# Performance work log

Measured on AMD Instinct MI355X. Metric: run time of the kernel, lower is better.

The kernel has to match this reference:

```python
import jax, jax.numpy as jnp
import numpy as np

N = 100_000       # nodes
E = 1_600_000     # directed edges (avg degree 16)
IN, H, Z = 128, 128, 64


def setup_inputs() -> dict:
    key = jax.random.key(0)
    ks = jax.random.split(key, 8)
    x = jax.random.normal(ks[0], (N, IN), dtype=jnp.float32)
    edge_index = jax.random.randint(ks[1], (2, E), 0, N, dtype=jnp.int32)
    # Glorot-ish init like PyG GCNConv
    W1 = jax.random.normal(ks[2], (IN, H), dtype=jnp.float32) / np.sqrt(IN).astype(np.float32)
    b1 = jnp.zeros((H,), dtype=jnp.float32)
    Wmu = jax.random.normal(ks[3], (H, Z), dtype=jnp.float32) / np.sqrt(H).astype(np.float32)
    bmu = jnp.zeros((Z,), dtype=jnp.float32)
    Wlv = jax.random.normal(ks[4], (H, Z), dtype=jnp.float32) / np.sqrt(H).astype(np.float32)
    blv = jnp.zeros((Z,), dtype=jnp.float32)
    return {"x": x, "edge_index": edge_index, "W1": W1, "b1": b1,
            "Wmu": Wmu, "bmu": bmu, "Wlv": Wlv, "blv": blv}


def _gcn_conv(x, src, dst, norm, W, b):
    """PyG GCNConv: out = scatter_add(norm * (x @ W)[src], dst) + b."""
    h = x @ W                                   # [N, out_dim]
    msg = h[src] * norm[:, None]                # [E+N, out_dim] gather + scale
    out = jax.ops.segment_sum(msg, dst, num_segments=N)
    return out + b


def reference(x, edge_index, W1, b1, Wmu, bmu, Wlv, blv):
    loop = jnp.arange(N, dtype=edge_index.dtype)
    src = jnp.concatenate([edge_index[0], loop])   # add self-loops (PyG default)
    dst = jnp.concatenate([edge_index[1], loop])
    # symmetric normalization D^{-1/2} (A+I) D^{-1/2}
    deg = jax.ops.segment_sum(jnp.ones_like(dst, dtype=x.dtype), dst, num_segments=N)
    dinv = jax.lax.rsqrt(deg)                      # deg >= 1 thanks to self-loops
    norm = dinv[src] * dinv[dst]                   # [E+N]
    h = jax.nn.relu(_gcn_conv(x, src, dst, norm, W1, b1))
    mu = _gcn_conv(h, src, dst, norm, Wmu, bmu)
    logvar = _gcn_conv(h, src, dst, norm, Wlv, blv)
    return (mu, logvar)
```

## Files before the change

kernel.cpp:

```cpp
#include <hip/hip_runtime.h>
#include <hip/hip_bf16.h>
#include <stdint.h>

static inline size_t ws_align(size_t x) { return (x + 255) & ~(size_t)255; }

typedef __attribute__((ext_vector_type(8))) short bf16x8;
typedef __attribute__((ext_vector_type(4))) float f32x4;

__device__ __forceinline__ uint32_t pack_bf16(float a, float b) {
    uint32_t ua = __float_as_uint(a), ub = __float_as_uint(b);
    ua = (ua + 0x7fffu + ((ua >> 16) & 1u)) >> 16;
    ub = (ub + 0x7fffu + ((ub >> 16) & 1u)) >> 16;
    return ua | (ub << 16);
}
__device__ __forceinline__ uint16_t cvt_bf16(float a) {
    uint32_t ua = __float_as_uint(a);
    return (uint16_t)((ua + 0x7fffu + ((ua >> 16) & 1u)) >> 16);
}
__device__ __forceinline__ float bf_lo(uint32_t v) { return __uint_as_float(v << 16); }
__device__ __forceinline__ float bf_hi(uint32_t v) { return __uint_as_float(v & 0xffff0000u); }

__device__ __forceinline__ void fma8(float* acc, uint4 g, float wt) {
    acc[0] = fmaf(bf_lo(g.x), wt, acc[0]); acc[1] = fmaf(bf_hi(g.x), wt, acc[1]);
    acc[2] = fmaf(bf_lo(g.y), wt, acc[2]); acc[3] = fmaf(bf_hi(g.y), wt, acc[3]);
    acc[4] = fmaf(bf_lo(g.z), wt, acc[4]); acc[5] = fmaf(bf_hi(g.z), wt, acc[5]);
    acc[6] = fmaf(bf_lo(g.w), wt, acc[6]); acc[7] = fmaf(bf_hi(g.w), wt, acc[7]);
}

__global__ __launch_bounds__(256) void k_pre(const int* __restrict__ dst, int* __restrict__ cntAB,
                                             const float* __restrict__ x, uint32_t* __restrict__ xb,
                                             const float* __restrict__ W1,
                                             const float* __restrict__ Wmu, const float* __restrict__ Wlv,
                                             uint32_t* __restrict__ BtG1, uint32_t* __restrict__ BtG2,
                                             int E, int nchunk, int NB, int n4) {
    const int b = blockIdx.x;
    if (b < nchunk) {
        __shared__ int h[512];
        for (int t = threadIdx.x; t < NB; t += 256) h[t] = 0;
        __syncthreads();
        const int per = (E + nchunk - 1) / nchunk;
        const int e0 = b * per, e1 = (e0 + per < E) ? e0 + per : E;
        for (int e = e0 + threadIdx.x; e < e1; e += 256)
            atomicAdd(&h[dst[e] >> 8], 1);
        __syncthreads();
        for (int t = threadIdx.x; t < NB; t += 256) cntAB[t * nchunk + b] = h[t];
    } else if (b < nchunk + 34) {
        int t = (b - nchunk) * 256 + threadIdx.x;
        int c = t / 68, k2 = t % 68;
        uint32_t v = 0;
        if (k2 < 64) v = pack_bf16(W1[(2 * k2) * 128 + c], W1[(2 * k2 + 1) * 128 + c]);
        BtG1[t] = v;
    } else if (b < nchunk + 68) {
        int t = (b - nchunk - 34) * 256 + threadIdx.x;
        int c = t / 68, k2 = t % 68;
        uint32_t v = 0;
        if (k2 < 64) {
            const float* Wc = (c < 64) ? (Wmu + c) : (Wlv + (c - 64));
            v = pack_bf16(Wc[(2 * k2) * 64], Wc[(2 * k2 + 1) * 64]);
        }
        BtG2[t] = v;
    } else {
        int idx = (b - nchunk - 68) * 256 + threadIdx.x;
        if (idx < n4) {
            float4 v = ((const float4*)x)[idx];
            ((uint2*)xb)[idx] = make_uint2(pack_bf16(v.x, v.y), pack_bf16(v.z, v.w));
        }
    }
}

__global__ __launch_bounds__(256) void k_scan1(const int* __restrict__ cnt, int* __restrict__ rp,
                                               int* __restrict__ bsum, int N) {
    __shared__ int sh[256];
    int t = threadIdx.x;
    int base = blockIdx.x * 1024 + t * 4;
    int v[4];
#pragma unroll
    for (int i = 0; i < 4; i++) v[i] = (base + i < N) ? cnt[base + i] : 0;
    int s = v[0] + v[1] + v[2] + v[3];
    sh[t] = s;
    __syncthreads();
    for (int off = 1; off < 256; off <<= 1) {
        int x = (t >= off) ? sh[t - off] : 0;
        __syncthreads();
        sh[t] += x;
        __syncthreads();
    }
    int excl = sh[t] - s;
    if (t == 255) bsum[blockIdx.x] = sh[255];
    int run = excl;
#pragma unroll
    for (int i = 0; i < 4; i++) {
        if (base + i < N) rp[base + i] = run;
        run += v[i];
    }
}

__global__ __launch_bounds__(256) void k_scan2(int* __restrict__ bsum, int nb) {
    __shared__ int sh[256];
    int t = threadIdx.x;
    int v = (t < nb) ? bsum[t] : 0;
    sh[t] = v;
    __syncthreads();
    for (int off = 1; off < 256; off <<= 1) {
        int x = (t >= off) ? sh[t - off] : 0;
        __syncthreads();
        sh[t] += x;
        __syncthreads();
    }
    if (t < nb) bsum[t] = sh[t] - v;
}

__global__ void k_scan3(int* __restrict__ rp, const int* __restrict__ bsum, int N, int E) {
    int i = blockIdx.x * blockDim.x + threadIdx.x;
    if (i < N) rp[i] += bsum[i >> 10];
    if (i == N) rp[N] = E;
}

__global__ __launch_bounds__(256) void k_bscatter(const int* __restrict__ src, const int* __restrict__ dst,
                                                  const int* __restrict__ baseAB, uint2* __restrict__ ebkt,
                                                  int E, int nchunk, int NB) {
    __shared__ int bump[512];
    const int c = blockIdx.x;
    for (int t = threadIdx.x; t < NB; t += 256) bump[t] = baseAB[t * nchunk + c];
    __syncthreads();
    const int per = (E + nchunk - 1) / nchunk;
    const int e0 = c * per, e1 = (e0 + per < E) ? e0 + per : E;
    for (int e = e0 + threadIdx.x; e < e1; e += 256) {
        int d = dst[e], s = src[e];
        int pos = atomicAdd(&bump[d >> 8], 1);
        ebkt[pos] = make_uint2((uint32_t)s, (uint32_t)d);
    }
}

__global__ __launch_bounds__(256) void k_bbuild(const uint2* __restrict__ ebkt, const int* __restrict__ baseAB,
                                                float* __restrict__ dinv, int* __restrict__ rp,
                                                uint32_t* __restrict__ csrc, int nchunk, int N) {
    __shared__ int h[256];
    __shared__ int sh[256];
    __shared__ int rpd[256];
    __shared__ int fl[256];
    const int t = threadIdx.x;
    h[t] = 0;
    fl[t] = 0;
    __syncthreads();
    const int b = blockIdx.x;
    const int e0 = baseAB[b * nchunk], e1 = baseAB[(b + 1) * nchunk];
    for (int e = e0 + t; e < e1; e += 256)
        atomicAdd(&h[ebkt[e].y & 255], 1);
    __syncthreads();
    const int c = h[t];
    sh[t] = c;
    __syncthreads();
    for (int off = 1; off < 256; off <<= 1) {
        int x = (t >= off) ? sh[t - off] : 0;
        __syncthreads();
        sh[t] += x;
        __syncthreads();
    }
    rpd[t] = e0 + sh[t] - c;
    int node = (b << 8) + t;
    if (node < N) {
        rp[node] = rpd[t];
        dinv[node] = rsqrtf((float)(c + 1));
    }
    if (node == N - 1 || t == 255) {
        if (node + 1 <= N && (node == N - 1)) rp[N] = e0 + sh[255];
    }
    __syncthreads();
    for (int e = e0 + t; e < e1; e += 256) {
        uint2 sd = ebkt[e];
        int dl = (int)(sd.y & 255);
        int posL = atomicAdd(&fl[dl], 1);
        csrc[rpd[dl] + posL] = sd.x;
    }
}

__global__ __launch_bounds__(256) void k_agg(const uint8_t* __restrict__ featB,
                                             uint32_t* __restrict__ outB,
                                             const int* __restrict__ rp,
                                             const uint32_t* __restrict__ csrc,
                                             const float* __restrict__ dinv, int N) {
    int node = blockIdx.x * 4 + (threadIdx.x >> 6);
    if (node >= N) return;
    int lane = threadIdx.x & 63;
    int j = lane & 15;
    int q = lane >> 4;
    int beg = rp[node], end = rp[node + 1];
    float di = dinv[node];
    float w0 = (q == 0) ? di * di : 0.0f;
    const uint8_t* fb = featB + (size_t)j * 16;

    uint4 sv = *(const uint4*)(fb + (size_t)node * 256);
    float acc[8];
    acc[0] = bf_lo(sv.x) * w0; acc[1] = bf_hi(sv.x) * w0;
    acc[2] = bf_lo(sv.y) * w0; acc[3] = bf_hi(sv.y) * w0;
    acc[4] = bf_lo(sv.z) * w0; acc[5] = bf_hi(sv.z) * w0;
    acc[6] = bf_lo(sv.w) * w0; acc[7] = bf_hi(sv.w) * w0;

    for (int base = beg + q; base < end; base += 16) {
        bool v1 = base + 4 < end, v2 = base + 8 < end, v3 = base + 12 < end;
        uint32_t s0 = csrc[base];
        uint32_t s1 = v1 ? csrc[base + 4] : 0u;
        uint32_t s2 = v2 ? csrc[base + 8] : 0u;
        uint32_t s3 = v3 ? csrc[base + 12] : 0u;
        float wa = dinv[s0] * di;
        float wb = v1 ? dinv[s1] * di : 0.f;
        float wc = v2 ? dinv[s2] * di : 0.f;
        float wd = v3 ? dinv[s3] * di : 0.f;
        uint4 g0 = *(const uint4*)(fb + (size_t)s0 * 256);
        uint4 g1 = *(const uint4*)(fb + (size_t)s1 * 256);
        uint4 g2 = *(const uint4*)(fb + (size_t)s2 * 256);
        uint4 g3 = *(const uint4*)(fb + (size_t)s3 * 256);
        fma8(acc, g0, wa);
        fma8(acc, g1, wb);
        fma8(acc, g2, wc);
        fma8(acc, g3, wd);
    }

#pragma unroll
    for (int k = 0; k < 8; k++) {
        acc[k] += __shfl_xor(acc[k], 16, 64);
        acc[k] += __shfl_xor(acc[k], 32, 64);
    }
    if (q == 0) {
        uint4 p = make_uint4(pack_bf16(acc[0], acc[1]), pack_bf16(acc[2], acc[3]),
                             pack_bf16(acc[4], acc[5]), pack_bf16(acc[6], acc[7]));
        *(uint4*)(outB + (size_t)node * 64 + j * 4) = p;
    }
}

__global__ __launch_bounds__(256) void k_gemm1_mfma(
        const uint8_t* __restrict__ A, uint8_t* __restrict__ C,
        const uint32_t* __restrict__ BtG, const float* __restrict__ bias, int N) {
    __shared__ uint32_t Bt[128 * 68];
    for (int t = threadIdx.x; t < 128 * 68 / 4; t += 256)
        ((uint4*)Bt)[t] = ((const uint4*)BtG)[t];
    __syncthreads();

    const int lane = threadIdx.x & 63;
    const int wv = threadIdx.x >> 6;
    const int rrow = lane & 15;
    const int g = lane >> 4;
    const int r0 = blockIdx.x * 64 + wv * 16;
    const int rl = r0 + rrow;
    const int rc = (rl < N) ? rl : (N - 1);

    bf16x8 a[4];
    const uint8_t* arow = A + (size_t)rc * 256 + g * 16;
#pragma unroll
    for (int kb = 0; kb < 4; kb++) a[kb] = *(const bf16x8*)(arow + kb * 64);

    f32x4 acc[8];
#pragma unroll
    for (int ct = 0; ct < 8; ct++) acc[ct] = (f32x4){0.f, 0.f, 0.f, 0.f};

    const char* btb = (const char*)Bt;
#pragma unroll
    for (int ct = 0; ct < 8; ct++) {
        const char* bp = btb + (ct * 16 + rrow) * 272 + g * 16;
#pragma unroll
        for (int kb = 0; kb < 4; kb++) {
            bf16x8 bfr = *(const bf16x8*)(bp + kb * 64);
            acc[ct] = __builtin_amdgcn_mfma_f32_16x16x32_bf16(a[kb], bfr, acc[ct], 0, 0, 0);
        }
    }

#pragma unroll
    for (int ct = 0; ct < 8; ct++) {
        const int col = ct * 16 + rrow;
        const float bv = bias[col];
#pragma unroll
        for (int r = 0; r < 4; r++) {
            int row = r0 + g * 4 + r;
            if (row < N) {
                float h = fmaxf(acc[ct][r] + bv, 0.f);
                *(uint16_t*)(C + (size_t)row * 256 + col * 2) = cvt_bf16(h);
            }
        }
    }
}

__global__ __launch_bounds__(256) void k_gemm2_mfma(
        const uint8_t* __restrict__ A, float* __restrict__ out,
        const uint32_t* __restrict__ BtG,
        const float* __restrict__ bmu, const float* __restrict__ blv, int N) {
    __shared__ uint32_t Bt[128 * 68];
    for (int t = threadIdx.x; t < 128 * 68 / 4; t += 256)
        ((uint4*)Bt)[t] = ((const uint4*)BtG)[t];
    __syncthreads();

    const int lane = threadIdx.x & 63;
    const int wv = threadIdx.x >> 6;
    const int rrow = lane & 15;
    const int g = lane >> 4;
    const int r0 = blockIdx.x * 64 + wv * 16;
    const int rl = r0 + rrow;
    const int rc = (rl < N) ? rl : (N - 1);

    bf16x8 a[4];
    const uint8_t* arow = A + (size_t)rc * 256 + g * 16;
#pragma unroll
    for (int kb = 0; kb < 4; kb++) a[kb] = *(const bf16x8*)(arow + kb * 64);

    f32x4 acc[8];
#pragma unroll
    for (int ct = 0; ct < 8; ct++) acc[ct] = (f32x4){0.f, 0.f, 0.f, 0.f};

    const char* btb = (const char*)Bt;
#pragma unroll
    for (int ct = 0; ct < 8; ct++) {
        const char* bp = btb + (ct * 16 + rrow) * 272 + g * 16;
#pragma unroll
        for (int kb = 0; kb < 4; kb++) {
            bf16x8 bfr = *(const bf16x8*)(bp + kb * 64);
            acc[ct] = __builtin_amdgcn_mfma_f32_16x16x32_bf16(a[kb], bfr, acc[ct], 0, 0, 0);
        }
    }

#pragma unroll
    for (int ct = 0; ct < 8; ct++) {
        const int col = ct * 16 + rrow;
        const float bv = (col < 64) ? bmu[col] : blv[col - 64];
        float* obase = (col < 64) ? (out + col) : (out + (size_t)N * 64 + (col - 64));
#pragma unroll
        for (int r = 0; r < 4; r++) {
            int row = r0 + g * 4 + r;
            if (row < N) obase[(size_t)row * 64] = acc[ct][r] + bv;
        }
    }
}

extern "C" void kernel_launch(void* const* d_in, const int* in_sizes, int n_in,
                              void* d_out, int out_size, void* d_ws, size_t ws_size,
                              hipStream_t stream) {
    const float* x   = (const float*)d_in[0];
    const int*   ei  = (const int*)d_in[1];
    const float* W1  = (const float*)d_in[2];
    const float* b1  = (const float*)d_in[3];
    const float* Wmu = (const float*)d_in[4];
    const float* bmu = (const float*)d_in[5];
    const float* Wlv = (const float*)d_in[6];
    const float* blv = (const float*)d_in[7];
    float* out = (float*)d_out;

    const int N = in_sizes[0] / 128;
    const int E = in_sizes[1] / 2;
    const int* src = ei;
    const int* dst = ei + E;

    const int nchunk = 256;
    const int NB = (N + 255) >> 8;
    const int M = NB * nchunk;
    const int n4 = N * 32;

    char* ws = (char*)d_ws;
    size_t off = 0;
    float* dinv    = (float*)(ws + off);    off = ws_align(off + (size_t)N * 4);
    int* rp        = (int*)(ws + off);      off = ws_align(off + (size_t)(N + 1) * 4);
    int* bsum      = (int*)(ws + off);      off = ws_align(off + 1024 * 4);
    int* cntAB     = (int*)(ws + off);      off = ws_align(off + (size_t)(M + 64) * 4);
    int* baseAB    = (int*)(ws + off);      off = ws_align(off + (size_t)(M + 64) * 4);
    uint32_t* BtG1 = (uint32_t*)(ws + off); off = ws_align(off + 128 * 68 * 4);
    uint32_t* BtG2 = (uint32_t*)(ws + off); off = ws_align(off + 128 * 68 * 4);
    uint32_t* csrc = (uint32_t*)(ws + off); off = ws_align(off + (size_t)E * 4);
    uint32_t* xb   = (uint32_t*)(ws + off); off = ws_align(off + (size_t)N * 256);
    uint8_t* F1    = (uint8_t*)(ws + off);  off = ws_align(off + (size_t)N * 256);
    uint2* ebkt    = (uint2*)(ws + off);    off = ws_align(off + (size_t)E * 8);

    const int b = 256;
    const int ncvt = (n4 + 255) / 256;

    k_pre<<<nchunk + 68 + ncvt, 256, 0, stream>>>(dst, cntAB, x, xb, W1, Wmu, Wlv,
                                                  BtG1, BtG2, E, nchunk, NB, n4);
    k_scan1<<<(M + 1023) / 1024, 256, 0, stream>>>(cntAB, baseAB, bsum, M);
    k_scan2<<<1, 256, 0, stream>>>(bsum, (M + 1023) / 1024);
    k_scan3<<<(M + 1 + b - 1) / b, b, 0, stream>>>(baseAB, bsum, M, E);
    k_bscatter<<<nchunk, 256, 0, stream>>>(src, dst, baseAB, ebkt, E, nchunk, NB);
    k_bbuild<<<NB, 256, 0, stream>>>(ebkt, baseAB, dinv, rp, csrc, nchunk, N);

    const int aggBlocks = (N + 3) / 4;
    k_agg<<<aggBlocks, 256, 0, stream>>>((const uint8_t*)xb, (uint32_t*)F1, rp, csrc, dinv, N);
    k_gemm1_mfma<<<(N + 63) / 64, 256, 0, stream>>>(F1, F1, BtG1, b1, N);

    k_agg<<<aggBlocks, 256, 0, stream>>>(F1, (uint32_t*)xb, rp, csrc, dinv, N);
    k_gemm2_mfma<<<(N + 63) / 64, 256, 0, stream>>>((const uint8_t*)xb, out, BtG2, bmu, blv, N);
}
```

Measured before the change: 223.8 us.

## Fold block-sum scan into consumers and pack edge bucket entries into 32 bits

Removes the separate k_scan2 and k_scan3 launches. Each k_bscatter and k_bbuild block now redundantly scans the small block-sum array in LDS and adds the offsets inline. The bucketed edge buffer is packed from 8-byte (src,dst) pairs into one 32-bit word, with the 24-bit source and the 8-bit local destination in the top byte. This halves scatter and gather traffic, but it assumes node ids fit in 24 bits and adds a small redundant scan to every block.

Result: no change. 221.7 us (-0.9%).

```diff
diff --git a/kernel.cpp b/kernel.cpp
--- a/kernel.cpp
+++ b/kernel.cpp
@@ -95,58 +95,65 @@
     }
 }
 
-__global__ __launch_bounds__(256) void k_scan2(int* __restrict__ bsum, int nb) {
-    __shared__ int sh[256];
-    int t = threadIdx.x;
+__device__ __forceinline__ void scan_bsum_lds(const int* __restrict__ bsum, int nb, int* bexc) {
+    const int t = threadIdx.x;
     int v = (t < nb) ? bsum[t] : 0;
-    sh[t] = v;
+    bexc[t] = v;
     __syncthreads();
     for (int off = 1; off < 256; off <<= 1) {
-        int x = (t >= off) ? sh[t - off] : 0;
-        __syncthreads();
-        sh[t] += x;
-        __syncthreads();
-    }
-    if (t < nb) bsum[t] = sh[t] - v;
-}
-
-__global__ void k_scan3(int* __restrict__ rp, const int* __restrict__ bsum, int N, int E) {
-    int i = blockIdx.x * blockDim.x + threadIdx.x;
-    if (i < N) rp[i] += bsum[i >> 10];
-    if (i == N) rp[N] = E;
+        int x = (t >= off) ? bexc[t - off] : 0;
+        __syncthreads();
+        bexc[t] += x;
+        __syncthreads();
+    }
+    int excl = bexc[t] - v;
+    __syncthreads();
+    bexc[t] = excl;
+    __syncthreads();
 }
 
 __global__ __launch_bounds__(256) void k_bscatter(const int* __restrict__ src, const int* __restrict__ dst,
-                                                  const int* __restrict__ baseAB, uint2* __restrict__ ebkt,
+                                                  const int* __restrict__ baseAB, const int* __restrict__ bsum,
+                                                  int nb, uint32_t* __restrict__ ebkt,
                                                   int E, int nchunk, int NB) {
     __shared__ int bump[512];
+    __shared__ int bexc[256];
+    scan_bsum_lds(bsum, nb, bexc);
     const int c = blockIdx.x;
-    for (int t = threadIdx.x; t < NB; t += 256) bump[t] = baseAB[t * nchunk + c];
+    for (int t = threadIdx.x; t < NB; t += 256) {
+        int idx = t * nchunk + c;
+        bump[t] = baseAB[idx] + bexc[idx >> 10];
+    }
     __syncthreads();
     const int per = (E + nchunk - 1) / nchunk;
     const int e0 = c * per, e1 = (e0 + per < E) ? e0 + per : E;
     for (int e = e0 + threadIdx.x; e < e1; e += 256) {
         int d = dst[e], s = src[e];
         int pos = atomicAdd(&bump[d >> 8], 1);
-        ebkt[pos] = make_uint2((uint32_t)s, (uint32_t)d);
-    }
-}
-
-__global__ __launch_bounds__(256) void k_bbuild(const uint2* __restrict__ ebkt, const int* __restrict__ baseAB,
-                                                float* __restrict__ dinv, int* __restrict__ rp,
-                                                uint32_t* __restrict__ csrc, int nchunk, int N) {
+        ebkt[pos] = (uint32_t)s | ((uint32_t)(d & 255) << 24);
+    }
+}
+
+__global__ __launch_bounds__(256) void k_bbuild(const uint32_t* __restrict__ ebkt,
+                                                const int* __restrict__ baseAB, const int* __restrict__ bsum,
+                                                int nb, float* __restrict__ dinv, int* __restrict__ rp,
+                                                uint32_t* __restrict__ csrc, int nchunk, int N, int E, int NB) {
     __shared__ int h[256];
     __shared__ int sh[256];
     __shared__ int rpd[256];
     __shared__ int fl[256];
+    __shared__ int bexc[256];
+    scan_bsum_lds(bsum, nb, bexc);
     const int t = threadIdx.x;
     h[t] = 0;
     fl[t] = 0;
     __syncthreads();
     const int b = blockIdx.x;
-    const int e0 = baseAB[b * nchunk], e1 = baseAB[(b + 1) * nchunk];
+    const int i0 = b * nchunk, i1 = (b + 1) * nchunk;
+    const int e0 = baseAB[i0] + bexc[i0 >> 10];
+    const int e1 = (i1 >= NB * nchunk) ? E : (baseAB[i1] + bexc[i1 >> 10]);
     for (int e = e0 + t; e < e1; e += 256)
-        atomicAdd(&h[ebkt[e].y & 255], 1);
+        atomicAdd(&h[ebkt[e] >> 24], 1);
     __syncthreads();
     const int c = h[t];
     sh[t] = c;
@@ -163,15 +170,13 @@
         rp[node] = rpd[t];
         dinv[node] = rsqrtf((float)(c + 1));
     }
-    if (node == N - 1 || t == 255) {
-        if (node + 1 <= N && (node == N - 1)) rp[N] = e0 + sh[255];
-    }
+    if (b == NB - 1 && t == 255) rp[N] = e0 + sh[255];
     __syncthreads();
     for (int e = e0 + t; e < e1; e += 256) {
-        uint2 sd = ebkt[e];
-        int dl = (int)(sd.y & 255);
+        uint32_t sd = ebkt[e];
+        int dl = (int)(sd >> 24);
         int posL = atomicAdd(&fl[dl], 1);
-        csrc[rpd[dl] + posL] = sd.x;
+        csrc[rpd[dl] + posL] = sd & 0x00ffffffu;
     }
 }
 
@@ -352,6 +357,7 @@
     const int NB = (N + 255) >> 8;
     const int M = NB * nchunk;
     const int n4 = N * 32;
+    const int nscan = (M + 1023) / 1024;
 
     char* ws = (char*)d_ws;
     size_t off = 0;
@@ -365,18 +371,15 @@
     uint32_t* csrc = (uint32_t*)(ws + off); off = ws_align(off + (size_t)E * 4);
     uint32_t* xb   = (uint32_t*)(ws + off); off = ws_align(off + (size_t)N * 256);
     uint8_t* F1    = (uint8_t*)(ws + off);  off = ws_align(off + (size_t)N * 256);
-    uint2* ebkt    = (uint2*)(ws + off);    off = ws_align(off + (size_t)E * 8);
-
-    const int b = 256;
+    uint32_t* ebkt = (uint32_t*)(ws + off); off = ws_align(off + (size_t)E * 4);
+
     const int ncvt = (n4 + 255) / 256;
 
     k_pre<<<nchunk + 68 + ncvt, 256, 0, stream>>>(dst, cntAB, x, xb, W1, Wmu, Wlv,
                                                   BtG1, BtG2, E, nchunk, NB, n4);
-    k_scan1<<<(M + 1023) / 1024, 256, 0, stream>>>(cntAB, baseAB, bsum, M);
-    k_scan2<<<1, 256, 0, stream>>>(bsum, (M + 1023) / 1024);
-    k_scan3<<<(M + 1 + b - 1) / b, b, 0, stream>>>(baseAB, bsum, M, E);
-    k_bscatter<<<nchunk, 256, 0, stream>>>(src, dst, baseAB, ebkt, E, nchunk, NB);
-    k_bbuild<<<NB, 256, 0, stream>>>(ebkt, baseAB, dinv, rp, csrc, nchunk, N);
+    k_scan1<<<nscan, 256, 0, stream>>>(cntAB, baseAB, bsum, M);
+    k_bscatter<<<nchunk, 256, 0, stream>>>(src, dst, baseAB, bsum, nscan, ebkt, E, nchunk, NB);
+    k_bbuild<<<NB, 256, 0, stream>>>(ebkt, baseAB, bsum, nscan, dinv, rp, csrc, nchunk, N, E, NB);
 
     const int aggBlocks = (N + 3) / 4;
     k_agg<<<aggBlocks, 256, 0, stream>>>((const uint8_t*)xb, (uint32_t*)F1, rp, csrc, dinv, N);
```
